# Optimization experiments

Measured on AMD Instinct MI355X. Metric: run time of the kernel, lower is better.

Reference implementation:

```python
import jax, jax.numpy as jnp
import numpy as np

B, H, W = 4, 256, 256
TARGET_BETA0 = 5
TARGET_LIFETIME = 0.5
LOSS_SCALE = 100.0


def setup_inputs() -> dict:
    key = jax.random.key(0)
    k1, k2 = jax.random.split(key)
    prob_map = jax.random.uniform(k1, (B, 1, H, W), dtype=jnp.float32)
    roi_mask = (jax.random.uniform(k2, (B, 1, H, W)) < 0.9).astype(jnp.float32)
    return {"prob_map": prob_map, "roi_mask": roi_mask}


def _ph0_topk_loss(f):
    """0-dim persistent homology (V-filtration, 4-connectivity) of f:[H,W],
    then standard top-k MSE(target_lifetime) loss. Equivalent to
    cripser.compute_ph_torch(f, maxdim=0, filtration='V') + _standard_loss.
    Algorithm: Kruskal over grid edges with weight max(f[u],f[v]), elder rule.
    All combinatorics run on stop_gradient values; births/deaths are
    differentiable gathers from f at the paired pixel indices."""
    Hh, Ww = f.shape
    N = Hh * Ww
    fv = f.reshape(-1)
    fvc = jax.lax.stop_gradient(fv)

    idx2d = jnp.arange(N, dtype=jnp.int32).reshape(Hh, Ww)
    r_u = idx2d[:, :-1].reshape(-1)  # right edges
    r_v = r_u + 1
    d_u = idx2d[:-1, :].reshape(-1)  # down edges
    d_v = d_u + Ww
    eu = jnp.concatenate([r_u, d_u])
    ev = jnp.concatenate([r_v, d_v])
    ew = jnp.maximum(fvc[eu], fvc[ev])
    order = jnp.argsort(ew)  # process edges by increasing filtration value
    eu, ev = eu[order], ev[order]

    parent0 = jnp.arange(N, dtype=jnp.int32)

    def step(parent, uv):
        u, v = uv[0], uv[1]

        def find(x):
            return jax.lax.while_loop(lambda y: parent[y] != y, lambda y: parent[y], x)

        ru = find(u)
        rv = find(v)
        merge = ru != rv
        # Invariant: a root is the argmin pixel of its component, so
        # fvc[root] is the component's birth value. Elder rule: the root
        # with smaller birth value survives (ties -> smaller index).
        older_u = (fvc[ru] < fvc[rv]) | ((fvc[ru] == fvc[rv]) & (ru < rv))
        keep = jnp.where(older_u, ru, rv)
        die = jnp.where(older_u, rv, ru)
        b_idx = jnp.where(merge, die, -1)  # birth pixel of the dying comp
        d_pix = jnp.where(fvc[u] >= fvc[v], u, v)  # death = max endpoint
        d_idx = jnp.where(merge, d_pix, -1)
        parent = parent.at[die].set(jnp.where(merge, keep, die))
        parent = parent.at[u].set(jnp.where(merge, keep, ru))  # path compression
        parent = parent.at[v].set(jnp.where(merge, keep, rv))
        return parent, (b_idx, d_idx)

    _, (pb, pd_) = jax.lax.scan(step, parent0, jnp.stack([eu, ev], axis=1))

    valid = pb >= 0
    births = fv[jnp.maximum(pb, 0)]
    deaths = fv[jnp.maximum(pd_, 0)]
    life = jnp.where(valid, deaths - births, 0.0)  # lifetimes >= 0

    # sort descending; invalid slots to the end (keys are stop-gradient)
    key_ = jnp.where(valid, jax.lax.stop_gradient(life), -jnp.inf)
    top = jnp.argsort(-key_)[:TARGET_BETA0]
    topk = life[top]
    vk = valid[top]
    n_use = jnp.sum(vk)  # = min(num_finite, target_beta0)
    sq = jnp.where(vk, (topk - TARGET_LIFETIME) ** 2, 0.0)
    return jnp.sum(sq) / jnp.maximum(n_use, 1).astype(f.dtype)


def reference(prob_map, roi_mask):
    prob = prob_map[:, 0] * roi_mask[:, 0]  # roi masking; (1-roi)*0 is a no-op
    filtration = 1.0 - prob
    losses = jax.vmap(_ph0_topk_loss)(filtration)
    return jnp.mean(losses) * LOSS_SCALE
```

## Files before the change

### kernel.cpp

```cpp
#include <hip/hip_runtime.h>
#include <stdint.h>

#define NPIX 65536
#define NRE  65280
#define NE   130560
#define NIMG 4
#define LTPB 1024
#define ETPB 1024
#define NBLK_L (NIMG*32)
#define TPIX 2048
#define EPAD 4096
#define KMAX 4096
#define HSZ  1024
#define LHSZ 2048
#define ECAP 4096
#define NCUT 2560
#define MTAILL 256
#define ETAIL  256
typedef unsigned long long u64;

__device__ __forceinline__ int ufind(unsigned* lbl, int x){
  int r = x, c = (int)lbl[r];
  while (c != r){ r = c; c = (int)lbl[r]; }
  while ((int)lbl[x] != r){ int n = (int)lbl[x]; lbl[x] = (unsigned)r; x = n; }
  return r;
}
__device__ __forceinline__ int ufind16(unsigned short* uf, int x){
  int r = x, c = (int)uf[r];
  while (c != r){ r = c; c = (int)uf[r]; }
  while ((int)uf[x] != r){ int n = (int)uf[x]; uf[x] = (unsigned short)r; x = n; }
  return r;
}

__device__ __forceinline__ void merge5(float* a, const float* b){
  float out[5]; int ia = 0, ib = 0;
  #pragma unroll
  for (int k = 0; k < 5; ++k){
    float av = (ia < 5) ? a[ia] : -2.0f;
    float bv = (ib < 5) ? b[ib] : -2.0f;
    if (av >= bv){ out[k] = av; ++ia; } else { out[k] = bv; ++ib; }
  }
  #pragma unroll
  for (int k = 0; k < 5; ++k) a[k] = out[k];
}

__device__ __forceinline__ void ins5(float* t5, float v){
  if (v > t5[4]){
    int j = 4;
    while (j > 0 && t5[j-1] < v){ t5[j] = t5[j-1]; --j; }
    t5[j] = v;
  }
}

__global__ __launch_bounds__(LTPB)
void ph0_local(const float* __restrict__ prob, const float* __restrict__ roi,
               float* __restrict__ LIFEg, unsigned* __restrict__ CIDg,
               u64* __restrict__ LAg,
               unsigned* __restrict__ C, unsigned* __restrict__ C2,
               unsigned* __restrict__ CUTWg, u64* __restrict__ RNKIg,
               float* __restrict__ T5g)
{
  const int blk = blockIdx.x;
  const int img = blk >> 5;
  const int tile = blk & 31;
  const int tr = tile >> 2, tc = tile & 3;
  const int gr0 = tr*32, gc0 = tc*64;
  const int tid = threadIdx.x;
  const int lane = tid & 63;

  const float* pm = prob + img*NPIX;
  const float* rm = roi  + img*NPIX;
  float* LIFE = LIFEg + img*NPIX;
  unsigned* CID = CIDg + img*NPIX;
  unsigned* CUTW = CUTWg + img*NCUT;
  u64* RNKI = RNKIg + (size_t)img*NPIX;
  u64* LA = LAg + (size_t)img*NE;

  __shared__ float          sf[TPIX];
  __shared__ unsigned       slbl[TPIX];
  __shared__ unsigned       smeb[2][TPIX];
  __shared__ float          slife[TPIX];
  __shared__ unsigned short el[2][EPAD];
  __shared__ unsigned       aux[EPAD];
  __shared__ unsigned       bkw[192];
  __shared__ unsigned short bkp[192];
  __shared__ unsigned       s_fired[TPIX/32];
  __shared__ float          s_t5w[(LTPB/64)*5];
  __shared__ int s_n[3];

  float t5[5] = {-1.f,-1.f,-1.f,-1.f,-1.f};

  for (int p = tid; p < TPIX; p += LTPB){
    int gp = ((gr0 + (p>>6))<<8) + gc0 + (p&63);
    float fv = 1.0f - pm[gp]*rm[gp];
    sf[p] = fv; slbl[p] = (unsigned)p;
    smeb[0][p] = 0xFFFFFFFFu; smeb[1][p] = 0xFFFFFFFFu;
    slife[p] = 0.0f;
  }
  if (tid < 3) s_n[tid] = 0;
  if (tid < TPIX/32) s_fired[tid] = 0;
  for (int s = tid; s < 192; s += LTPB){
    unsigned wv = 0xFFFFFFFFu; int p = 0; int gq = -1;
    if (s < 32){ if (tc > 0){ p = s*64;        gq = ((gr0+s)<<8)    + gc0 - 1;  } }
    else if (s < 64){ int k=s-32;  if (tc < 3){ p = k*64+63;  gq = ((gr0+k)<<8)  + gc0 + 64; } }
    else if (s < 128){ int k=s-64; if (tr > 0){ p = k;        gq = ((gr0-1)<<8)  + gc0 + k;  } }
    else { int k=s-128;            if (tr < 7){ p = 31*64+k;  gq = ((gr0+32)<<8) + gc0 + k;  } }
    if (gq >= 0){
      int gp = ((gr0 + (p>>6))<<8) + gc0 + (p&63);
      float fp = 1.0f - pm[gp]*rm[gp];
      float fq = 1.0f - pm[gq]*rm[gq];
      wv = __float_as_uint(fmaxf(fp, fq));
    }
    bkw[s] = wv; bkp[s] = (unsigned short)p;
  }
  __syncthreads();

  if (tid < 192){
    int s = tid;
    if (s >= 32 && s < 64  && tc < 3) CUTW[(tc<<8) | (gr0 + (s-32))] = bkw[s];
    if (s >= 128           && tr < 7) CUTW[768 + (tr<<8) + (gc0 + (s-128))] = bkw[s];
  }

  int M = EPAD, cur = 0, rd = 0;
  bool tailm = false;
  for (; rd < 100000; ++rd){
    int nxt = cur ^ 1;
    unsigned* sme  = smeb[rd & 1];
    unsigned* smeN = smeb[(rd+1) & 1];
    int bs = tid - (LTPB - 192);
    if (bs >= 0){
      unsigned wv = bkw[bs];
      if (wv != 0xFFFFFFFFu) atomicMin(&sme[ufind(slbl, (int)bkp[bs])], wv);
    }
    int Mpad = (M + 63) & ~63;
    for (int idx = tid; idx < Mpad; idx += LTPB){
      bool keep = false; int e=0,u=0,v=0,a=0,b=0;
      if (idx < M){
        e = (rd == 0) ? idx : (int)el[cur][idx];
        bool valid;
        if (e < 2048){ u=e; v=e+1; valid = ((e&63)!=63); }
        else { u=e-2048; v=u+64; valid = ((u>>6)!=31); }
        if (valid){
          a = ufind(slbl,u); b = ufind(slbl,v);
          if (a != b){
            unsigned wb = __float_as_uint(fmaxf(sf[u],sf[v]));
            atomicMin(&sme[a],wb); atomicMin(&sme[b],wb);
            keep = true;
          }
        }
      }
      u64 m = __ballot(keep);
      if (m){
        int pos0 = __popcll(m & ((1ULL<<lane)-1));
        int leader = __ffsll((long long)m)-1;
        int base = 0;
        if (lane == leader) base = atomicAdd(&s_n[rd%3], __popcll(m));
        base = __shfl(base, leader);
        if (keep){
          el[nxt][base+pos0] = (unsigned short)e;
          aux[base+pos0] = (unsigned)a | ((unsigned)b<<16);
        }
      }
    }
    __syncthreads();
    int n = s_n[rd%3];
    cur = nxt;
    if (n == M || n == 0){ M = n; break; }
    M = n;
    for (int idx = tid; idx < M; idx += LTPB){
      int e = (int)el[cur][idx];
      unsigned ab = aux[idx];
      int a = (int)(ab & 0xFFFFu), b = (int)(ab >> 16);
      int u, v;
      if (e < 2048){ u = e; v = e + 1; } else { u = e - 2048; v = u + 64; }
      float w = fmaxf(sf[u], sf[v]);
      unsigned wb = __float_as_uint(w);
      float fa = sf[a], fb = sf[b];
      bool bd = (fb < fa) || ((fb == fa) && (b < a));
      int die = bd ? a : b, keep = bd ? b : a;
      if (sme[die] == wb){
        slbl[die] = (unsigned)keep;
        float lt = w - (bd ? fa : fb);
        slife[die] = lt;
        unsigned bbit = 1u << (die & 31);
        if (!(atomicOr(&s_fired[die >> 5], bbit) & bbit)) ins5(t5, lt);
      }
      smeN[a] = 0xFFFFFFFFu; smeN[b] = 0xFFFFFFFFu;
    }
    if (tid == 0) s_n[(rd+1)%3] = 0;
    __syncthreads();
    if (M <= MTAILL){ ++rd; tailm = true; break; }
  }

  if (tailm){
    if (tid < 64){
      for (;; ++rd){
        unsigned* sme  = smeb[rd & 1];
        unsigned* smeN = smeb[(rd+1) & 1];
        for (int s = lane; s < 192; s += 64){
          unsigned wv = bkw[s];
          if (wv != 0xFFFFFFFFu) atomicMin(&sme[ufind(slbl, (int)bkp[s])], wv);
        }
        __builtin_amdgcn_wave_barrier();
        int nxt = cur ^ 1;
        int nacc = 0;
        for (int i0 = 0; i0 < M; i0 += 64){
          int idx = i0 + lane;
          bool keep = false; int e = 0, a = 0, b = 0;
          if (idx < M){
            e = (int)el[cur][idx];
            int u, v;
            if (e < 2048){ u = e; v = e + 1; } else { u = e - 2048; v = u + 64; }
            a = ufind(slbl,u); b = ufind(slbl,v);
            if (a != b){
              unsigned wb = __float_as_uint(fmaxf(sf[u],sf[v]));
              atomicMin(&sme[a],wb); atomicMin(&sme[b],wb);
              keep = true;
            }
          }
          u64 mm = __ballot(keep);
          if (keep){
            int pos = nacc + __popcll(mm & ((1ULL<<lane)-1));
            el[nxt][pos] = (unsigned short)e;
            aux[pos] = (unsigned)a | ((unsigned)b<<16);
          }
          nacc += __popcll(mm);
        }
        __builtin_amdgcn_wave_barrier();
        int n = nacc;
        cur = nxt;
        if (n == M || n == 0){ M = n; break; }
        M = n;
        for (int i0 = 0; i0 < M; i0 += 64){
          int idx = i0 + lane;
          if (idx < M){
            int e = (int)el[cur][idx];
            unsigned ab = aux[idx];
            int a = (int)(ab & 0xFFFFu), b = (int)(ab >> 16);
            int u, v;
            if (e < 2048){ u = e; v = e + 1; } else { u = e - 2048; v = u + 64; }
            float w = fmaxf(sf[u], sf[v]);
            unsigned wb = __float_as_uint(w);
            float fa = sf[a], fb = sf[b];
            bool bd = (fb < fa) || ((fb == fa) && (b < a));
            int die = bd ? a : b, kp = bd ? b : a;
            if (sme[die] == wb){
              slbl[die] = (unsigned)kp;
              float lt = w - (bd ? fa : fb);
              slife[die] = lt;
              unsigned bbit = 1u << (die & 31);
              if (!(atomicOr(&s_fired[die >> 5], bbit) & bbit)) ins5(t5, lt);
            }
            smeN[a] = 0xFFFFFFFFu; smeN[b] = 0xFFFFFFFFu;
          }
        }
        __builtin_amdgcn_wave_barrier();
      }
      if (lane == 0){ s_n[0] = M; s_n[1] = cur; }
    }
    __syncthreads();
    M = s_n[0]; cur = s_n[1];
  }

  unsigned* posm = smeb[0];
  for (int p = tid; p < TPIX; p += LTPB){
    if ((int)slbl[p] == p){
      unsigned pos = atomicAdd(&C2[img], 1u);
      posm[p] = pos;
      unsigned gp = (unsigned)(((gr0 + (p>>6))<<8) + gc0 + (p&63));
      RNKI[pos] = ((u64)__float_as_uint(sf[p]) << 32) | gp;
    }
  }
  __syncthreads();
  for (int p = tid; p < TPIX; p += LTPB){
    int r = ufind(slbl, p);
    int gp = ((gr0 + (p>>6))<<8) + gc0 + (p&63);
    CID[gp] = posm[r];
    LIFE[gp] = slife[p];
  }
  __syncthreads();

  unsigned* hk = (unsigned*)&el[cur ^ 1][0];
  unsigned* hw = slbl;
  for (int i = tid; i < LHSZ; i += LTPB){ hk[i] = 0xFFFFFFFFu; hw[i] = 0xFFFFFFFFu; }
  __syncthreads();

  unsigned* ctr = &C[img];
  int Mpad2 = (M + 63) & ~63;
  for (int idx = tid; idx < Mpad2; idx += LTPB){
    bool spill = false;
    u64 rec = 0;
    if (idx < M){
      int e = (int)el[cur][idx];
      unsigned ab = aux[idx];
      int a = (int)(ab & 0xFFFFu), b = (int)(ab >> 16);
      int u, v;
      if (e < 2048){ u = e; v = e + 1; } else { u = e - 2048; v = u + 64; }
      unsigned wb = __float_as_uint(fmaxf(sf[u], sf[v]));
      int lo = a < b ? a : b, hi = a < b ? b : a;
      unsigned key = ((unsigned)lo << 11) | (unsigned)hi;
      unsigned h = ((key * 2654435761u) >> 21) & (LHSZ-1);
      bool ins = false;
      #pragma unroll
      for (int t = 0; t < 8; ++t){
        unsigned old = atomicCAS(&hk[h], 0xFFFFFFFFu, key);
        if (old == 0xFFFFFFFFu || old == key){ atomicMin(&hw[h], wb); ins = true; break; }
        h = (h + 1) & (LHSZ-1);
      }
      if (!ins){
        spill = true;
        rec = ((u64)wb << 32) | ((u64)posm[a] << 16) | posm[b];
      }
    }
    u64 m = __ballot(spill);
    if (m){
      int pos0 = __popcll(m & ((1ULL<<lane)-1));
      int leader = __ffsll((long long)m)-1;
      unsigned base = 0;
      if (lane == leader) base = atomicAdd(ctr, (unsigned)__popcll(m));
      base = (unsigned)__shfl((int)base, leader);
      if (spill) LA[base + pos0] = rec;
    }
  }
  __syncthreads();
  for (int h = tid; h < LHSZ; h += LTPB){
    unsigned key = hk[h];
    bool ok = (key != 0xFFFFFFFFu);
    u64 rec = 0;
    if (ok){
      int a = (int)(key >> 11), b = (int)(key & 0x7FFu);
      rec = ((u64)hw[h] << 32) | ((u64)posm[a] << 16) | posm[b];
    }
    u64 m = __ballot(ok);
    if (m){
      int pos0 = __popcll(m & ((1ULL<<lane)-1));
      int leader = __ffsll((long long)m)-1;
      unsigned base = 0;
      if (lane == leader) base = atomicAdd(ctr, (unsigned)__popcll(m));
      base = (unsigned)__shfl((int)base, leader);
      if (ok) LA[base + pos0] = rec;
    }
  }

  #pragma unroll
  for (int off = 1; off < 64; off <<= 1){
    float o[5];
    #pragma unroll
    for (int k = 0; k < 5; ++k) o[k] = __shfl_xor(t5[k], off);
    merge5(t5, o);
  }
  if (lane == 0){
    int wv = tid >> 6;
    #pragma unroll
    for (int k = 0; k < 5; ++k) s_t5w[wv*5+k] = t5[k];
  }
  __syncthreads();
  if (tid < 64){
    float u5[5];
    #pragma unroll
    for (int k = 0; k < 5; ++k) u5[k] = (tid < LTPB/64) ? s_t5w[tid*5+k] : -2.0f;
    #pragma unroll
    for (int off = 1; off < 16; off <<= 1){
      float o[5];
      #pragma unroll
      for (int k = 0; k < 5; ++k) o[k] = __shfl_xor(u5[k], off);
      merge5(u5, o);
    }
    if (tid == 0){
      #pragma unroll
      for (int k = 0; k < 5; ++k) T5g[blk*5+k] = u5[k];
    }
  }
}

#define RUN_ROUNDS_GLOBAL(UF, ME, RNK)                                       \
  for (int k = tid; k < K; k += ETPB) UF[k] = (unsigned short)k;             \
  __syncthreads();                                                           \
  for (int rdg = 0; rdg < 70000 && n > 0; ++rdg){                            \
    for (int k = tid; k < K; k += ETPB) ME[k] = 0xFFFFFFFFu;                 \
    if (tid == 0) s_n[0] = 0;                                                \
    __syncthreads();                                                         \
    int Mpad = (n + 63) & ~63;                                               \
    for (int idx = tid; idx < Mpad; idx += ETPB){                            \
      bool keep = false; unsigned wb = 0; int a = 0, b = 0;                  \
      if (idx < n){                                                          \
        u64 rec = src[idx];                                                  \
        wb = (unsigned)(rec >> 32);                                          \
        a = (int)((rec >> 16) & 0xFFFFu);                                    \
        b = (int)(rec & 0xFFFFu);                                            \
        a = ufind16(UF, a); b = ufind16(UF, b);                              \
        if (a != b){ atomicMin(&ME[a], wb); atomicMin(&ME[b], wb); keep = true; } \
      }                                                                      \
      u64 m = __ballot(keep);                                                \
      if (m){                                                                \
        int pos0 = __popcll(m & ((1ULL<<lane)-1));                           \
        int leader = __ffsll((long long)m)-1;                                \
        int base = 0;                                                        \
        if (lane == leader) base = atomicAdd(&s_n[0], __popcll(m));          \
        base = __shfl(base, leader);                                         \
        if (keep) dst[base+pos0] = ((u64)wb<<32)|((u64)(unsigned)a<<16)|(unsigned)b; \
      }                                                                      \
    }                                                                        \
    __syncthreads();                                                         \
    int nn = s_n[0];                                                         \
    for (int idx = tid; idx < nn; idx += ETPB){                              \
      u64 rec = dst[idx];                                                    \
      unsigned wb = (unsigned)(rec >> 32);                                   \
      int a = (int)((rec >> 16) & 0xFFFFu);                                  \
      int b = (int)(rec & 0xFFFFu);                                          \
      bool bd = RNK[b] < RNK[a];                                             \
      int die = bd ? a : b, kp = bd ? b : a;                                 \
      if (ME[die] == wb){                                                    \
        UF[die] = (unsigned short)kp;                                        \
        u64 rk = RNK[die];                                                   \
        life[(unsigned)(rk & 0xFFFFFFFFu)] =                                 \
            __uint_as_float(wb) - __uint_as_float((unsigned)(rk >> 32));     \
      }                                                                      \
    }                                                                        \
    __syncthreads();                                                         \
    u64* t = src; src = dst; dst = t; n = nn;                                \
  }

__global__ __launch_bounds__(ETPB)
void ph0_endgame(float* __restrict__ LIFEg, unsigned* __restrict__ CIDg,
                 const unsigned* __restrict__ CUTWg, u64* __restrict__ RNKIg,
                 u64* __restrict__ LAg, u64* __restrict__ LBg,
                 const unsigned* __restrict__ C, const unsigned* __restrict__ C2,
                 const float* __restrict__ T5g,
                 float* __restrict__ LOSS, unsigned* __restrict__ DONE,
                 float* __restrict__ out)
{
  const int img = blockIdx.x, tid = threadIdx.x;
  const int lane = tid & 63;
  float* life = LIFEg + img*NPIX;
  unsigned* cid = CIDg + img*NPIX;
  const unsigned* cw = CUTWg + img*NCUT;
  u64* RNKI = RNKIg + (size_t)img*NPIX;
  u64* src = LAg + (size_t)img*NE;
  u64* dst = LBg + (size_t)img*NE;

  __shared__ unsigned short s_uf[KMAX];
  __shared__ unsigned s_meB[2*KMAX];
  __shared__ unsigned s_hkB[2*HSZ];
  __shared__ unsigned s_hwB[2*HSZ];
  __shared__ u64 s_rnk[KMAX];
  __shared__ u64 s_lstA[ECAP];
  __shared__ u64 s_lstB[ECAP];
  __shared__ unsigned s_fired[KMAX/32];
  __shared__ float s_w5[(ETPB/64)*5];
  __shared__ int s_n[3];

  const int K = (int)C2[img];
  const int nInt = (int)C[img];

  for (int s = tid; s < NCUT; s += ETPB){
    int gu, gv;
    if (s < 768){ int ci = s >> 8, row = s & 255, col = 63 + (ci<<6); gu = (row<<8)+col; gv = gu+1; }
    else { int k = s - 768; int ri = k >> 8, colh = k & 255, gr = 31 + (ri<<5); gu = (gr<<8)+colh; gv = gu+256; }
    unsigned ia = cid[gu];
    unsigned ib = cid[gv];
    unsigned wb = cw[s];
    s_lstA[s] = ((u64)wb << 32) | ((u64)ia << 16) | ib;
  }
  if (tid < 3) s_n[tid] = 0;
  int n = nInt + NCUT;

  float t5[5] = {-1.f,-1.f,-1.f,-1.f,-1.f};

  if (K <= KMAX){
    for (int k = tid; k < K; k += ETPB){
      s_uf[k] = (unsigned short)k;
      s_rnk[k] = RNKI[k];
      s_meB[k] = 0xFFFFFFFFu;
    }
    for (int h = tid; h < HSZ; h += ETPB){ s_hkB[h] = 0xFFFFFFFFu; s_hwB[h] = 0xFFFFFFFFu; }
    if (tid < KMAX/32) s_fired[tid] = 0;
    if (tid < 32*5) ins5(t5, T5g[img*(32*5) + tid]);
    __syncthreads();

    u64 *lsrc = s_lstA, *ldst = s_lstB;
    int rd = 0; bool tailm = false;

    for (; rd < 70000; ++rd){
      const int bi = rd & 1;
      unsigned* me  = s_meB + bi*KMAX;
      unsigned* meN = s_meB + (bi^1)*KMAX;
      unsigned* hk = s_hkB + bi*HSZ;
      unsigned* hw = s_hwB + bi*HSZ;
      const bool useHash = (n > 1024);
      int Mpad = (n + 63) & ~63;
      for (int idx = tid; idx < Mpad; idx += ETPB){
        bool app = false; unsigned wb = 0; int a = 0, b = 0;
        if (idx < n){
          u64 rec;
          if (rd == 0) rec = (idx < NCUT) ? lsrc[idx] : src[idx - NCUT];
          else         rec = (idx < ECAP) ? lsrc[idx] : src[idx];
          a = (int)((rec >> 16) & 0xFFFFu);
          b = (int)(rec & 0xFFFFu);
          a = ufind16(s_uf, a); b = ufind16(s_uf, b);
          if (a != b){
            wb = (unsigned)(rec >> 32);
            if (useHash){
              int lo = a < b ? a : b, hi = a < b ? b : a;
              unsigned key = ((unsigned)lo << 12) | (unsigned)hi;
              unsigned h = ((key * 2654435761u) >> 20) & (HSZ-1);
              bool ins = false;
              #pragma unroll
              for (int t = 0; t < 8; ++t){
                unsigned old = atomicCAS(&hk[h], 0xFFFFFFFFu, key);
                if (old == 0xFFFFFFFFu || old == key){ atomicMin(&hw[h], wb); ins = true; break; }
                h = (h + 1) & (HSZ-1);
              }
              if (!ins){ atomicMin(&me[a], wb); atomicMin(&me[b], wb); app = true; }
            } else {
              atomicMin(&me[a], wb); atomicMin(&me[b], wb); app = true;
            }
          }
        }
        u64 m = __ballot(app);
        if (m){
          int pos0 = __popcll(m & ((1ULL<<lane)-1));
          int leader = __ffsll((long long)m)-1;
          int base = 0;
          if (lane == leader) base = atomicAdd(&s_n[rd%3], __popcll(m));
          base = __shfl(base, leader);
          if (app){
            u64 r = ((u64)wb<<32)|((u64)(unsigned)a<<16)|(unsigned)b;
            int pos = base+pos0;
            if (pos < ECAP) ldst[pos] = r; else dst[pos] = r;
          }
        }
      }
      __syncthreads();
      if (useHash){
        for (int h = tid; h < HSZ; h += ETPB){
          unsigned key = hk[h];
          bool okk = (key != 0xFFFFFFFFu);
          unsigned wb = 0; int a = 0, b = 0;
          if (okk){
            a = (int)(key >> 12); b = (int)(key & 0xFFFu);
            wb = hw[h];
            atomicMin(&me[a], wb); atomicMin(&me[b], wb);
          }
          u64 m = __ballot(okk);
          if (m){
            int pos0 = __popcll(m & ((1ULL<<lane)-1));
            int leader = __ffsll((long long)m)-1;
            int base = 0;
            if (lane == leader) base = atomicAdd(&s_n[rd%3], __popcll(m));
            base = __shfl(base, leader);
            if (okk){
              u64 r = ((u64)wb<<32)|((u64)(unsigned)a<<16)|(unsigned)b;
              int pos = base+pos0;
              if (pos < ECAP) ldst[pos] = r; else dst[pos] = r;
            }
          }
        }
        __syncthreads();
      }
      int nn = s_n[rd%3];
      if (nn == 0) break;
      for (int idx = tid; idx < nn; idx += ETPB){
        u64 rec = (idx < ECAP) ? ldst[idx] : dst[idx];
        unsigned wb = (unsigned)(rec >> 32);
        int a = (int)((rec >> 16) & 0xFFFFu);
        int b = (int)(rec & 0xFFFFu);
        u64 ra = s_rnk[a], rb = s_rnk[b];
        bool bd = rb < ra;
        int die = bd ? a : b, kp = bd ? b : a;
        if (me[die] == wb){
          s_uf[die] = (unsigned short)kp;
          unsigned bbit = 1u << (die & 31);
          if (!(atomicOr(&s_fired[die >> 5], bbit) & bbit)){
            u64 rk = bd ? ra : rb;
            ins5(t5, __uint_as_float(wb) - __uint_as_float((unsigned)(rk >> 32)));
          }
        }
        meN[a] = 0xFFFFFFFFu; meN[b] = 0xFFFFFFFFu;
      }
      if (nn > 1024){
        unsigned* hkN = s_hkB + (bi^1)*HSZ;
        unsigned* hwN = s_hwB + (bi^1)*HSZ;
        for (int h = tid; h < HSZ; h += ETPB){ hkN[h] = 0xFFFFFFFFu; hwN[h] = 0xFFFFFFFFu; }
      }
      if (tid == 0) s_n[(rd+1)%3] = 0;
      __syncthreads();
      { u64* t = src; src = dst; dst = t; }
      { u64* t2 = lsrc; lsrc = ldst; ldst = t2; }
      n = nn;
      if (n <= ETAIL){ ++rd; tailm = true; break; }
    }

    if (tailm){
      if (tid < 64){
        for (;; ++rd){
          const int bi = rd & 1;
          unsigned* me  = s_meB + bi*KMAX;
          unsigned* meN = s_meB + (bi^1)*KMAX;
          int nacc = 0;
          for (int i0 = 0; i0 < n; i0 += 64){
            int idx = i0 + lane;
            bool app = false; unsigned wb = 0; int a = 0, b = 0;
            if (idx < n){
              u64 rec = lsrc[idx];
              a = (int)((rec >> 16) & 0xFFFFu);
              b = (int)(rec & 0xFFFFu);
              a = ufind16(s_uf, a); b = ufind16(s_uf, b);
              if (a != b){
                wb = (unsigned)(rec >> 32);
                atomicMin(&me[a], wb); atomicMin(&me[b], wb);
                app = true;
              }
            }
            u64 mm = __ballot(app);
            if (app){
              int pos = nacc + __popcll(mm & ((1ULL<<lane)-1));
              ldst[pos] = ((u64)wb<<32)|((u64)(unsigned)a<<16)|(unsigned)b;
            }
            nacc += __popcll(mm);
          }
          __builtin_amdgcn_wave_barrier();
          int nn = nacc;
          if (nn == 0) break;
          for (int i0 = 0; i0 < nn; i0 += 64){
            int idx = i0 + lane;
            if (idx < nn){
              u64 rec = ldst[idx];
              unsigned wb = (unsigned)(rec >> 32);
              int a = (int)((rec >> 16) & 0xFFFFu);
              int b = (int)(rec & 0xFFFFu);
              u64 ra = s_rnk[a], rb = s_rnk[b];
              bool bd = rb < ra;
              int die = bd ? a : b, kp = bd ? b : a;
              if (me[die] == wb){
                s_uf[die] = (unsigned short)kp;
                unsigned bbit = 1u << (die & 31);
                if (!(atomicOr(&s_fired[die >> 5], bbit) & bbit)){
                  u64 rk = bd ? ra : rb;
                  ins5(t5, __uint_as_float(wb) - __uint_as_float((unsigned)(rk >> 32)));
                }
              }
              meN[a] = 0xFFFFFFFFu; meN[b] = 0xFFFFFFFFu;
            }
          }
          __builtin_amdgcn_wave_barrier();
          { u64* t2 = lsrc; lsrc = ldst; ldst = t2; }
          n = nn;
        }
      }
      __syncthreads();
    }
  } else {
    __syncthreads();
    for (int s = tid; s < NCUT; s += ETPB) src[nInt + s] = s_lstA[s];
    __syncthreads();
    unsigned short* g_uf = (unsigned short*)cid;
    unsigned*       g_me = (unsigned*)(cid + NPIX/2);
    u64*            g_rnk = RNKI;
    RUN_ROUNDS_GLOBAL(g_uf, g_me, g_rnk)
    for (int i = tid; i < NPIX; i += ETPB) ins5(t5, life[i]);
  }

  #pragma unroll
  for (int off = 1; off < 64; off <<= 1){
    float o[5];
    #pragma unroll
    for (int k = 0; k < 5; ++k) o[k] = __shfl_xor(t5[k], off);
    merge5(t5, o);
  }
  if (lane == 0){
    int wv = tid >> 6;
    #pragma unroll
    for (int k = 0; k < 5; ++k) s_w5[wv*5+k] = t5[k];
  }
  __syncthreads();
  if (tid < 64){
    float u5[5];
    #pragma unroll
    for (int k = 0; k < 5; ++k) u5[k] = (tid < ETPB/64) ? s_w5[tid*5+k] : -2.0f;
    #pragma unroll
    for (int off = 1; off < 16; off <<= 1){
      float o[5];
      #pragma unroll
      for (int k = 0; k < 5; ++k) o[k] = __shfl_xor(u5[k], off);
      merge5(u5, o);
    }
    if (tid == 0){
      float lsum = 0.0f;
      #pragma unroll
      for (int k = 0; k < 5; ++k){ float d = u5[k] - 0.5f; lsum += d*d; }
      atomicExch(&LOSS[img], lsum * 0.2f);
      __threadfence();
      unsigned prev = atomicAdd(DONE, 1u);
      if (prev == NIMG - 1){
        float s = 0.0f;
        #pragma unroll
        for (int i = 0; i < NIMG; ++i) s += atomicAdd(&LOSS[i], 0.0f);
        out[0] = s * 25.0f;
      }
    }
  }
}

extern "C" void kernel_launch(void* const* d_in, const int* in_sizes, int n_in,
                              void* d_out, int out_size, void* d_ws, size_t ws_size,
                              hipStream_t stream)
{
  const float* prob = (const float*)d_in[0];
  const float* roi  = (const float*)d_in[1];
  char* ws = (char*)d_ws;
  const size_t SZL = (size_t)4*NE*8;
  float*    LIFE = (float*)(ws + (1u<<20));
  unsigned* CID  = (unsigned*)(ws + (2u<<20));
  unsigned* CUTW = (unsigned*)(ws + (3u<<20));
  u64*      LA   = (u64*)(ws + (5u<<20));
  u64*      LB   = (u64*)(ws + (5u<<20) + SZL);
  u64*      RNKI = (u64*)(ws + (5u<<20) + 2*SZL);
  unsigned* C    = (unsigned*)(ws + (5u<<20) + 2*SZL + (2u<<20));
  unsigned* C2   = C + 4;
  unsigned* DONE = C + 8;
  float*    LOSS = (float*)((char*)C + 64);
  float*    T5   = (float*)(ws + (5u<<20) + 2*SZL - 2560);
  float*    out  = (float*)d_out;

  hipMemsetAsync(C, 0, 64, stream);
  ph0_local<<<NBLK_L, LTPB, 0, stream>>>(prob, roi, LIFE, CID, LA, C, C2, CUTW, RNKI, T5);
  ph0_endgame<<<NIMG, ETPB, 0, stream>>>(LIFE, CID, CUTW, RNKI, LA, LB, C, C2, T5, LOSS, DONE, out);
}
```

Measured before the change: 258.7 us.

## Track per-component boundary minimum incrementally instead of rescanning boundary edges each round

Adds a per-root shared array holding the minimum weight of tile-crossing boundary edges. Each round, only the roots that died in the previous round push their value to their new root via a compacted fired list. Before, all 192 boundary edges ran a union-find and an atomicMin into the candidate-minimum array every round. The fire test now also checks the boundary minimum against the edge weight. This cuts repeated finds on boundary pixels but adds extra shared memory, ballot-based list compaction and a second atomicMin per merge.

```diff
diff --git a/kernel.cpp b/kernel.cpp
--- a/kernel.cpp
+++ b/kernel.cpp
@@ -2,7 +2,6 @@
 #include <stdint.h>
 
 #define NPIX 65536
-#define NRE  65280
 #define NE   130560
 #define NIMG 4
 #define LTPB 1024
@@ -80,13 +79,16 @@
   __shared__ unsigned       slbl[TPIX];
   __shared__ unsigned       smeb[2][TPIX];
   __shared__ float          slife[TPIX];
+  __shared__ unsigned       blkm[TPIX];
   __shared__ unsigned short el[2][EPAD];
   __shared__ unsigned       aux[EPAD];
+  __shared__ unsigned short fdl[2][EPAD];
   __shared__ unsigned       bkw[192];
   __shared__ unsigned short bkp[192];
   __shared__ unsigned       s_fired[TPIX/32];
   __shared__ float          s_t5w[(LTPB/64)*5];
   __shared__ int s_n[3];
+  __shared__ int s_fd[2];
 
   float t5[5] = {-1.f,-1.f,-1.f,-1.f,-1.f};
 
@@ -95,9 +97,11 @@
     float fv = 1.0f - pm[gp]*rm[gp];
     sf[p] = fv; slbl[p] = (unsigned)p;
     smeb[0][p] = 0xFFFFFFFFu; smeb[1][p] = 0xFFFFFFFFu;
+    blkm[p] = 0xFFFFFFFFu;
     slife[p] = 0.0f;
   }
   if (tid < 3) s_n[tid] = 0;
+  if (tid < 2) s_fd[tid] = 0;
   if (tid < TPIX/32) s_fired[tid] = 0;
   for (int s = tid; s < 192; s += LTPB){
     unsigned wv = 0xFFFFFFFFu; int p = 0; int gq = -1;
@@ -119,6 +123,7 @@
     int s = tid;
     if (s >= 32 && s < 64  && tc < 3) CUTW[(tc<<8) | (gr0 + (s-32))] = bkw[s];
     if (s >= 128           && tr < 7) CUTW[768 + (tr<<8) + (gc0 + (s-128))] = bkw[s];
+    if (bkw[s] != 0xFFFFFFFFu) atomicMin(&blkm[(int)bkp[s]], bkw[s]);
   }
 
   int M = EPAD, cur = 0, rd = 0;
@@ -127,10 +132,13 @@
     int nxt = cur ^ 1;
     unsigned* sme  = smeb[rd & 1];
     unsigned* smeN = smeb[(rd+1) & 1];
-    int bs = tid - (LTPB - 192);
-    if (bs >= 0){
-      unsigned wv = bkw[bs];
-      if (wv != 0xFFFFFFFFu) atomicMin(&sme[ufind(slbl, (int)bkp[bs])], wv);
+    {
+      int pv = (rd & 1) ^ 1;
+      int fc = s_fd[pv];
+      for (int i = tid; i < fc; i += LTPB){
+        int d = (int)fdl[pv][i];
+        atomicMin(&blkm[ufind(slbl, d)], blkm[d]);
+      }
     }
     int Mpad = (M + 63) & ~63;
     for (int idx = tid; idx < Mpad; idx += LTPB){
@@ -178,16 +186,28 @@
       float fa = sf[a], fb = sf[b];
       bool bd = (fb < fa) || ((fb == fa) && (b < a));
       int die = bd ? a : b, keep = bd ? b : a;
-      if (sme[die] == wb){
+      bool fire = false;
+      if (sme[die] == wb && blkm[die] >= wb){
+        fire = true;
         slbl[die] = (unsigned)keep;
         float lt = w - (bd ? fa : fb);
         slife[die] = lt;
+        atomicMin(&blkm[keep], blkm[die]);
         unsigned bbit = 1u << (die & 31);
         if (!(atomicOr(&s_fired[die >> 5], bbit) & bbit)) ins5(t5, lt);
       }
       smeN[a] = 0xFFFFFFFFu; smeN[b] = 0xFFFFFFFFu;
-    }
-    if (tid == 0) s_n[(rd+1)%3] = 0;
+      u64 fm = __ballot(fire);
+      if (fm){
+        int pos0 = __popcll(fm & ((1ULL<<lane)-1));
+        int leader = __ffsll((long long)fm)-1;
+        int base2 = 0;
+        if (lane == leader) base2 = atomicAdd(&s_fd[rd&1], __popcll(fm));
+        base2 = __shfl(base2, leader);
+        if (fire) fdl[rd&1][base2+pos0] = (unsigned short)die;
+      }
+    }
+    if (tid == 0){ s_n[(rd+1)%3] = 0; s_fd[(rd&1)^1] = 0; }
     __syncthreads();
     if (M <= MTAILL){ ++rd; tailm = true; break; }
   }
@@ -197,9 +217,13 @@
       for (;; ++rd){
         unsigned* sme  = smeb[rd & 1];
         unsigned* smeN = smeb[(rd+1) & 1];
-        for (int s = lane; s < 192; s += 64){
-          unsigned wv = bkw[s];
-          if (wv != 0xFFFFFFFFu) atomicMin(&sme[ufind(slbl, (int)bkp[s])], wv);
+        {
+          int pv = (rd & 1) ^ 1;
+          int fc = s_fd[pv];
+          for (int i = lane; i < fc; i += 64){
+            int d = (int)fdl[pv][i];
+            atomicMin(&blkm[ufind(slbl, d)], blkm[d]);
+          }
         }
         __builtin_amdgcn_wave_barrier();
         int nxt = cur ^ 1;
@@ -231,8 +255,10 @@
         cur = nxt;
         if (n == M || n == 0){ M = n; break; }
         M = n;
+        int fdc = 0;
         for (int i0 = 0; i0 < M; i0 += 64){
           int idx = i0 + lane;
+          bool fire = false; int die = 0;
           if (idx < M){
             int e = (int)el[cur][idx];
             unsigned ab = aux[idx];
@@ -243,17 +269,27 @@
             unsigned wb = __float_as_uint(w);
             float fa = sf[a], fb = sf[b];
             bool bd = (fb < fa) || ((fb == fa) && (b < a));
-            int die = bd ? a : b, kp = bd ? b : a;
-            if (sme[die] == wb){
+            die = bd ? a : b;
+            int kp = bd ? b : a;
+            if (sme[die] == wb && blkm[die] >= wb){
+              fire = true;
               slbl[die] = (unsigned)kp;
               float lt = w - (bd ? fa : fb);
               slife[die] = lt;
+              atomicMin(&blkm[kp], blkm[die]);
               unsigned bbit = 1u << (die & 31);
               if (!(atomicOr(&s_fired[die >> 5], bbit) & bbit)) ins5(t5, lt);
             }
             smeN[a] = 0xFFFFFFFFu; smeN[b] = 0xFFFFFFFFu;
           }
-        }
+          u64 fm = __ballot(fire);
+          if (fire){
+            int pos = fdc + __popcll(fm & ((1ULL<<lane)-1));
+            fdl[rd&1][pos] = (unsigned short)die;
+          }
+          fdc += __popcll(fm);
+        }
+        if (lane == 0){ s_fd[rd&1] = fdc; s_fd[(rd&1)^1] = 0; }
         __builtin_amdgcn_wave_barrier();
       }
       if (lane == 0){ s_n[0] = M; s_n[1] = cur; }
```

Measured after the change: 263.0 us. No clear change (+1.7%).
